# Performance work log

Measured on AMD Instinct MI355X. Metric: run time of the kernel, lower is better.

Reference implementation:

```python
import jax, jax.numpy as jnp
import numpy as np
from jax import lax

# Model config (matches init_kwargs)
D = 256          # input_size
DO = 256         # output_size
H = 512          # hidden_size
E = 8            # num_experts
NB = 4           # num_bands
R = 8            # lora_rank
ALPHA = 16.0     # lora_alpha
CAP_F = 1.25     # capacity_factor
F = 64           # dct_freq_features
N = 65536        # num tokens
CAP = int(CAP_F * N / E)  # 10240 tokens per expert (expert-choice capacity)


def setup_inputs() -> dict:
    key = jax.random.key(0)
    ks = jax.random.split(key, 14)
    s = 0.02
    return {
        "x": jax.random.normal(ks[0], (N, D), jnp.float32),
        "band": jax.random.randint(ks[1], (N,), 0, NB, jnp.int32),
        "W_dct": jax.random.normal(ks[2], (D, F), jnp.float32) * s,
        "W_gate": jax.random.normal(ks[3], (D + F, E), jnp.float32) * s,
        "W1": jax.random.normal(ks[4], (E, D + 1, H), jnp.float32) * s,
        "b1": jnp.zeros((E, H), jnp.float32),
        "A1": jax.random.normal(ks[5], (E, NB, D + 1, R), jnp.float32) * s,
        "B1": jax.random.normal(ks[6], (E, NB, R, H), jnp.float32) * s,
        "W2": jax.random.normal(ks[7], (E, H, DO), jnp.float32) * s,
        "b2": jnp.zeros((E, DO), jnp.float32),
        "A2": jax.random.normal(ks[8], (E, NB, H, R), jnp.float32) * s,
        "B2": jax.random.normal(ks[9], (E, NB, R, DO), jnp.float32) * s,
    }


def reference(x, band, W_dct, W_gate, W1, b1, A1, B1, W2, b2, A2, B2):
    scale = ALPHA / R
    # 1) Frequency-aware gating: concat spatial + (linear) DCT-like features.
    freq = x @ W_dct                                   # [N,F]
    logits = jnp.concatenate([x, freq], -1) @ W_gate   # [N,E]
    # Expert-choice: softmax over the TOKEN axis, each expert picks top-CAP tokens.
    scores = jax.nn.softmax(logits, axis=0)            # [N,E]
    g, idx = lax.top_k(scores.T, CAP)                  # [E,CAP] weights / token ids
    # 2) Dispatch: gather tokens (band scalar appended -> input_size+1 features).
    band_f = band.astype(x.dtype)[:, None] / NB        # [N,1]
    x_full = jnp.concatenate([x, band_f], -1)          # [N,D+1]
    xe = x_full[idx]                                   # [E,CAP,D+1]
    oh = jax.nn.one_hot(band[idx], NB, dtype=x.dtype)  # [E,CAP,NB]
    ohn = jnp.transpose(oh, (0, 2, 1))[..., None]      # [E,NB,CAP,1]
    # 3) Per-expert shared MLP with per-band LoRA adapters (layer 1).
    h = jnp.einsum('ecd,edh->ech', xe, W1) + b1[:, None, :]
    u = jnp.einsum('ecd,endr->encr', xe, A1) * ohn     # band-select low-rank code
    h = h + scale * jnp.einsum('encr,enrh->ech', u, B1)
    h = jax.nn.gelu(h)
    # Layer 2.
    o = jnp.einsum('ech,eho->eco', h, W2) + b2[:, None, :]
    v = jnp.einsum('ech,enhr->encr', h, A2) * ohn
    o = o + scale * jnp.einsum('encr,enro->eco', v, B2)
    # 4) Combine: scatter-add gate-weighted expert outputs (unselected tokens -> 0).
    y = jnp.zeros((N, DO), x.dtype)
    y = y.at[idx.reshape(-1)].add((g[..., None] * o).reshape(-1, DO))
    return y
```

## Files before the change

### kernel.cpp

```cpp
#include <hip/hip_runtime.h>
#include <hip/hip_bf16.h>
#include <math.h>

#define NTOK 65536
#define DIN 256
#define DOUT 256
#define HID 512
#define NEXP 8
#define NBAND 4
#define RANK 8
#define CAP 10240
#define NTILE 64
#define TILES_PER_E (CAP / NTILE)

#define W1CAT_PER_E (34 * 9 * 512)
#define B1CAT_OFF   (NEXP * W1CAT_PER_E)
#define B1CAT_PER_E (32 * 512)
#define W2CAT_OFF   (B1CAT_OFF + NEXP * B1CAT_PER_E)
#define W2CAT_PER_E (18 * 16 * 512)
#define B2CAT_OFF   (W2CAT_OFF + NEXP * W2CAT_PER_E)
#define B2CAT_PER_E (16 * 512)
#define PK_TOTAL    (B2CAT_OFF + NEXP * B2CAT_PER_E)
#define PK_F32_OFF  1200000

typedef short s16x8 __attribute__((ext_vector_type(8)));
typedef float f32x4 __attribute__((ext_vector_type(4)));

__device__ __forceinline__ unsigned key_of(float f) {
    unsigned u = __float_as_uint(f);
    return (u & 0x80000000u) ? ~u : (u | 0x80000000u);
}
__device__ __forceinline__ float gelu_fast(float v) {
    const float c = 0.7978845608028654f;
    float z = c * (v + 0.044715f * v * v * v);
    float e = __expf(2.0f * z);
    return v * (1.0f - __builtin_amdgcn_rcpf(e + 1.0f));
}
__device__ __forceinline__ ushort f2bf(float f) {
    unsigned u = __float_as_uint(f);
    return (ushort)((u + 0x7FFFu + ((u >> 16) & 1u)) >> 16);
}

__global__ __launch_bounds__(256) void k_foldw(const float* __restrict__ Wdct,
                                               const float* __restrict__ Wgate,
                                               float* __restrict__ weff) {
    int d = threadIdx.x;
    float acc[8];
#pragma unroll
    for (int e = 0; e < 8; ++e) acc[e] = Wgate[d * 8 + e];
    for (int f = 0; f < 64; ++f) {
        float wv = Wdct[d * 64 + f];
#pragma unroll
        for (int e = 0; e < 8; ++e) acc[e] += wv * Wgate[(256 + f) * 8 + e];
    }
#pragma unroll
    for (int e = 0; e < 8; ++e) weff[d * 8 + e] = acc[e];
}

__global__ __launch_bounds__(256) void k_logits(const float* __restrict__ x,
                                                const float* __restrict__ weff,
                                                float* __restrict__ logitsT,
                                                float* __restrict__ partials) {
    __shared__ float pr[4][8];
    int tid = threadIdx.x, w = tid >> 6, lane = tid & 63;
    int wid = blockIdx.x * 4 + w;
    int nbase = wid * 16;
    float4 wa[4], wb[4];
#pragma unroll
    for (int j = 0; j < 4; ++j) {
        const float* wr = weff + (lane * 4 + j) * 8;
        wa[j] = *(const float4*)wr;
        wb[j] = *(const float4*)(wr + 4);
    }
    float es = 0.f;
    for (int t = 0; t < 16; ++t) {
        int n = nbase + t;
        float4 v = *(const float4*)(x + (size_t)n * DIN + lane * 4);
        float acc[8];
#pragma unroll
        for (int e = 0; e < 8; ++e) acc[e] = 0.f;
#pragma unroll
        for (int j = 0; j < 4; ++j) {
            float vj = (j == 0) ? v.x : (j == 1) ? v.y : (j == 2) ? v.z : v.w;
            acc[0] += vj * wa[j].x; acc[1] += vj * wa[j].y;
            acc[2] += vj * wa[j].z; acc[3] += vj * wa[j].w;
            acc[4] += vj * wb[j].x; acc[5] += vj * wb[j].y;
            acc[6] += vj * wb[j].z; acc[7] += vj * wb[j].w;
        }
#pragma unroll
        for (int off = 1; off < 64; off <<= 1) {
#pragma unroll
            for (int e = 0; e < 8; ++e) acc[e] += __shfl_xor(acc[e], off);
        }
        float out = acc[0];
#pragma unroll
        for (int e = 1; e < 8; ++e) if (lane == e) out = acc[e];
        if (lane < 8) {
            logitsT[(size_t)lane * NTOK + n] = out;
            es += expf(out);
        }
    }
    if (lane < 8) pr[w][lane] = es;
    __syncthreads();
    if (tid < 8) partials[(size_t)tid * 1024 + blockIdx.x] =
        pr[0][tid] + pr[1][tid] + pr[2][tid] + pr[3][tid];
}

__global__ __launch_bounds__(1024) void k_topk(const float* __restrict__ logitsT,
                                               const float* __restrict__ partials,
                                               float* __restrict__ colsum,
                                               int* __restrict__ idxbuf) {
    __shared__ unsigned subh[16][257];
    __shared__ unsigned bins[256];
    __shared__ float ssum[16];
    __shared__ unsigned sval[2];
    __shared__ unsigned scnt, stcnt;
    __shared__ int ties_l[2048];
    int e = blockIdx.x, tid = threadIdx.x, w = tid >> 6, lane = tid & 63;
    const float* lp = logitsT + (size_t)e * NTOK;

    {
        float s = partials[(size_t)e * 1024 + tid];
#pragma unroll
        for (int off = 32; off > 0; off >>= 1) s += __shfl_xor(s, off);
        if (lane == 0) ssum[w] = s;
        __syncthreads();
        if (tid == 0) {
            float t = 0.f;
#pragma unroll
            for (int i = 0; i < 16; ++i) t += ssum[i];
            colsum[e] = t;
        }
    }

    unsigned pref = 0, rem = CAP;
    for (int p = 0; p < 4; ++p) {
        int shift = 24 - 8 * p;
        for (int i = tid; i < 16 * 257; i += 1024) ((unsigned*)subh)[i] = 0;
        __syncthreads();
        for (int it = 0; it < 64; ++it) {
            int n = it * 1024 + tid;
            unsigned k = key_of(lp[n]);
            bool ok = (p == 0) || ((k >> (shift + 8)) == pref);
            if (ok) atomicAdd(&subh[w][(k >> shift) & 255u], 1u);
        }
        __syncthreads();
        if (tid < 256) {
            unsigned c = 0;
#pragma unroll
            for (int ww = 0; ww < 16; ++ww) c += subh[ww][tid];
            bins[tid] = c;
        }
        __syncthreads();
        for (int off = 1; off < 256; off <<= 1) {
            unsigned add = (tid < 256 && tid + off < 256) ? bins[tid + off] : 0u;
            __syncthreads();
            if (tid < 256) bins[tid] += add;
            __syncthreads();
        }
        if (tid < 256) {
            unsigned snext = (tid == 255) ? 0u : bins[tid + 1];
            if (bins[tid] >= rem && snext < rem) {
                sval[0] = (pref << 8) | (unsigned)tid;
                sval[1] = rem - snext;
            }
        }
        __syncthreads();
        pref = sval[0];
        rem = sval[1];
        __syncthreads();
    }

    if (tid == 0) { scnt = 0; stcnt = 0; }
    __syncthreads();
    unsigned T = pref;
    for (int it = 0; it < 64; ++it) {
        int n = it * 1024 + tid;
        unsigned k = key_of(lp[n]);
        if (k > T) {
            unsigned pos = atomicAdd(&scnt, 1u);
            idxbuf[e * CAP + pos] = n;
        } else if (k == T) {
            unsigned tp = atomicAdd(&stcnt, 1u);
            if (tp < 2048) ties_l[tp] = n;
        }
    }
    __syncthreads();
    int m = (int)stcnt, r = (int)rem, base = CAP - r;
    if (m == r) {
        for (int i = tid; i < m; i += 1024) idxbuf[e * CAP + base + i] = ties_l[i];
    } else {
        for (int i = tid; i < m; i += 1024) {
            int my = ties_l[i];
            int rank = 0;
            for (int j = 0; j < m; ++j) rank += (ties_l[j] < my);
            if (rank < r) idxbuf[e * CAP + base + rank] = my;
        }
    }
}

__global__ __launch_bounds__(256) void k_prep(const float* __restrict__ W1,
                                              const float* __restrict__ A1,
                                              const float* __restrict__ B1,
                                              const float* __restrict__ W2,
                                              const float* __restrict__ A2,
                                              const float* __restrict__ B2,
                                              ushort* __restrict__ pk) {
    int id = blockIdx.x * 256 + threadIdx.x;
    if (id >= PK_TOTAL) return;
    float val;
    if (id < B1CAT_OFF) {
        int e = id / W1CAT_PER_E, rem = id % W1CAT_PER_E;
        int t = rem / (9 * 512); rem %= 9 * 512;
        int s = rem / 512; int q = rem & 511;
        int l = q >> 3, j = q & 7;
        int k = s * 32 + ((l >> 4) << 3) + j;
        int col = t * 16 + (l & 15);
        if (k > 256) val = 0.f;
        else if (col < 512) val = W1[((size_t)e * 257 + k) * 512 + col];
        else {
            int cu = col - 512;
            val = A1[(((size_t)e * NBAND + (cu >> 3)) * 257 + k) * RANK + (cu & 7)];
        }
    } else if (id < W2CAT_OFF) {
        int id2 = id - B1CAT_OFF;
        int e = id2 / B1CAT_PER_E, rem = id2 % B1CAT_PER_E;
        int t = rem / 512; int q = rem & 511;
        int l = q >> 3, j = q & 7;
        int k32 = ((l >> 4) << 3) + j;
        int col = t * 16 + (l & 15);
        val = 2.0f * B1[(((size_t)e * NBAND + (k32 >> 3)) * RANK + (k32 & 7)) * 512 + col];
    } else if (id < B2CAT_OFF) {
        int id2 = id - W2CAT_OFF;
        int e = id2 / W2CAT_PER_E, rem = id2 % W2CAT_PER_E;
        int t = rem / (16 * 512); rem %= 16 * 512;
        int s = rem / 512; int q = rem & 511;
        int l = q >> 3, j = q & 7;
        int k = s * 32 + ((l >> 4) << 3) + j;
        int col = t * 16 + (l & 15);
        if (col < 256) val = W2[((size_t)e * 512 + k) * 256 + col];
        else {
            int cv = col - 256;
            val = A2[(((size_t)e * NBAND + (cv >> 3)) * 512 + k) * RANK + (cv & 7)];
        }
    } else {
        int id2 = id - B2CAT_OFF;
        int e = id2 / B2CAT_PER_E, rem = id2 % B2CAT_PER_E;
        int t = rem / 512; int q = rem & 511;
        int l = q >> 3, j = q & 7;
        int k32 = ((l >> 4) << 3) + j;
        int col = t * 16 + (l & 15);
        val = 2.0f * B2[(((size_t)e * NBAND + (k32 >> 3)) * RANK + (k32 & 7)) * 256 + col];
    }
    pk[id] = f2bf(val);
}

__global__ __launch_bounds__(256, 2) void k_expert(
    const float* __restrict__ x, const int* __restrict__ band,
    const float* __restrict__ b1, const float* __restrict__ b2,
    const ushort* __restrict__ pk,
    const float* __restrict__ logitsT,
    const float* __restrict__ colsum, const int* __restrict__ idxbuf,
    float* __restrict__ y) {
    __shared__ ushort bW1[9216];
    __shared__ ushort bW2[9216];
    __shared__ ushort sc[4][640];
    __shared__ int s_tok[4][16];
    __shared__ int s_band[4][16];
    __shared__ float s_g[4][16];

    int tid = threadIdx.x, w = tid >> 6, lane = tid & 63;
    int bid = blockIdx.x;
    int e = bid & 7;
    int tile = bid >> 3;

    if (lane < 16) {
        int n = idxbuf[e * CAP + tile * NTILE + w * 16 + lane];
        s_tok[w][lane] = n;
        s_band[w][lane] = band[n];
        s_g[w][lane] = expf(logitsT[(size_t)e * NTOK + n]) / colsum[e];
    }

    int l15 = lane & 15, lg = lane >> 4;
    ushort* scw = &sc[w][0];

    s16x8 a1[9];
    {
        int mytok = s_tok[w][l15];
        const float* xrow = x + (size_t)mytok * DIN;
        int kg = lg << 3;
#pragma unroll
        for (int s = 0; s < 8; ++s) {
            float4 p = *(const float4*)&xrow[s * 32 + kg];
            float4 q = *(const float4*)&xrow[s * 32 + kg + 4];
            s16x8 a;
            a[0] = (short)f2bf(p.x); a[1] = (short)f2bf(p.y);
            a[2] = (short)f2bf(p.z); a[3] = (short)f2bf(p.w);
            a[4] = (short)f2bf(q.x); a[5] = (short)f2bf(q.y);
            a[6] = (short)f2bf(q.z); a[7] = (short)f2bf(q.w);
            a1[s] = a;
        }
        s16x8 a = (s16x8)(short)0;
        if (lane < 16) a[0] = (short)f2bf((float)s_band[w][l15] * 0.25f);
        a1[8] = a;
    }

    const ushort* w1base = pk + (size_t)e * W1CAT_PER_E;
    const ushort* b1base = pk + B1CAT_OFF + (size_t)e * B1CAT_PER_E;
    const ushort* w2base = pk + W2CAT_OFF + (size_t)e * W2CAT_PER_E;
    const ushort* b2base = pk + B2CAT_OFF + (size_t)e * B2CAT_PER_E;

    s16x8 stg[9];
    if (w < 2) {
        const ushort* s0 = w2base + (size_t)(w * 9) * 16 * 512 + lane * 8;
#pragma unroll
        for (int i = 0; i < 9; ++i)
            stg[i] = *(const s16x8*)(s0 + (size_t)i * 16 * 512);
    } else {
        const ushort* s0 = w1base + (size_t)(w - 2) * 9 * 512 + lane * 8;
#pragma unroll
        for (int i = 0; i < 9; ++i)
            stg[i] = *(const s16x8*)(s0 + i * 512);
    }

    s16x8 ufrag;
    {
#pragma unroll
        for (int t = 32; t <= 33; ++t) {
            f32x4 acc = {0.f, 0.f, 0.f, 0.f};
#pragma unroll
            for (int s = 0; s < 9; ++s) {
                s16x8 b = *(const s16x8*)(w1base + ((size_t)t * 9 + s) * 512 + lane * 8);
                acc = __builtin_amdgcn_mfma_f32_16x16x32_bf16(a1[s], b, acc, 0, 0, 0);
            }
            int colbase = (t - 32) * 16 + l15;
#pragma unroll
            for (int r = 0; r < 4; ++r) {
                int row = lg * 4 + r;
                float v = ((colbase >> 3) == s_band[w][row]) ? acc[r] : 0.f;
                scw[row * 40 + colbase] = f2bf(v);
            }
        }
        asm volatile("s_waitcnt lgkmcnt(0)" ::: "memory");
        __builtin_amdgcn_sched_barrier(0);
        ufrag = *(const s16x8*)&scw[l15 * 40 + lg * 8];
    }

    f32x4 oacc[16];
#pragma unroll
    for (int t2 = 0; t2 < 16; ++t2) {
        float bv = b2[(size_t)e * DOUT + t2 * 16 + l15];
        oacc[t2] = (f32x4){bv, bv, bv, bv};
    }
    f32x4 vacc[2];
    vacc[0] = (f32x4){0.f, 0.f, 0.f, 0.f};
    vacc[1] = (f32x4){0.f, 0.f, 0.f, 0.f};

    if (w < 2) {
#pragma unroll
        for (int i = 0; i < 9; ++i)
            *(s16x8*)(&bW2[(w * 9 + i) * 512] + lane * 8) = stg[i];
    } else {
#pragma unroll
        for (int i = 0; i < 9; ++i)
            *(s16x8*)(&bW1[((w - 2) * 9 + i) * 512] + lane * 8) = stg[i];
    }
    __syncthreads();

#pragma unroll 1
    for (int p = 0; p < 16; ++p) {
        s16x8 st2[9];
        if (p < 15) {
            int p1 = p + 1;
            if (w < 2) {
                const ushort* s0 = w2base + ((size_t)(w * 9) * 16 + p1) * 512 + lane * 8;
#pragma unroll
                for (int i = 0; i < 9; ++i)
                    st2[i] = *(const s16x8*)(s0 + (size_t)i * 16 * 512);
            } else {
                int t = p1 * 2 + (w - 2);
                const ushort* s0 = w1base + (size_t)t * 9 * 512 + lane * 8;
#pragma unroll
                for (int i = 0; i < 9; ++i)
                    st2[i] = *(const s16x8*)(s0 + i * 512);
            }
        }
#pragma unroll
        for (int half = 0; half < 2; ++half) {
            int t = p * 2 + half;
            float bv = b1[(size_t)e * HID + t * 16 + l15];
            f32x4 acc = {bv, bv, bv, bv};
#pragma unroll
            for (int s = 0; s < 9; ++s) {
                s16x8 b = *(const s16x8*)(&bW1[(half * 9 + s) * 512] + lane * 8);
                acc = __builtin_amdgcn_mfma_f32_16x16x32_bf16(a1[s], b, acc, 0, 0, 0);
            }
            {
                s16x8 b = *(const s16x8*)(b1base + (size_t)t * 512 + lane * 8);
                acc = __builtin_amdgcn_mfma_f32_16x16x32_bf16(ufrag, b, acc, 0, 0, 0);
            }
#pragma unroll
            for (int r = 0; r < 4; ++r) {
                int row = lg * 4 + r;
                scw[row * 40 + half * 16 + l15] = f2bf(gelu_fast(acc[r]));
            }
        }
        asm volatile("s_waitcnt lgkmcnt(0)" ::: "memory");
        __builtin_amdgcn_sched_barrier(0);
        s16x8 hfrag = *(const s16x8*)&scw[l15 * 40 + lg * 8];
#pragma unroll
        for (int t2 = 0; t2 < 16; ++t2) {
            s16x8 b = *(const s16x8*)(&bW2[t2 * 512] + lane * 8);
            oacc[t2] = __builtin_amdgcn_mfma_f32_16x16x32_bf16(hfrag, b, oacc[t2], 0, 0, 0);
        }
#pragma unroll
        for (int i = 0; i < 2; ++i) {
            s16x8 b = *(const s16x8*)(&bW2[(16 + i) * 512] + lane * 8);
            vacc[i] = __builtin_amdgcn_mfma_f32_16x16x32_bf16(hfrag, b, vacc[i], 0, 0, 0);
        }
        if (p < 15) {
            __syncthreads();
            if (w < 2) {
#pragma unroll
                for (int i = 0; i < 9; ++i)
                    *(s16x8*)(&bW2[(w * 9 + i) * 512] + lane * 8) = st2[i];
            } else {
#pragma unroll
                for (int i = 0; i < 9; ++i)
                    *(s16x8*)(&bW1[((w - 2) * 9 + i) * 512] + lane * 8) = st2[i];
            }
            __syncthreads();
        }
    }

    s16x8 vfrag;
    {
#pragma unroll
        for (int i = 0; i < 2; ++i) {
            int colbase = i * 16 + l15;
#pragma unroll
            for (int r = 0; r < 4; ++r) {
                int row = lg * 4 + r;
                float v = ((colbase >> 3) == s_band[w][row]) ? vacc[i][r] : 0.f;
                scw[row * 40 + colbase] = f2bf(v);
            }
        }
        asm volatile("s_waitcnt lgkmcnt(0)" ::: "memory");
        __builtin_amdgcn_sched_barrier(0);
        vfrag = *(const s16x8*)&scw[l15 * 40 + lg * 8];
    }

    float g4[4];
    int tok4[4];
#pragma unroll
    for (int r = 0; r < 4; ++r) {
        int row = lg * 4 + r;
        g4[r] = s_g[w][row];
        tok4[r] = s_tok[w][row];
    }
#pragma unroll
    for (int t2 = 0; t2 < 16; ++t2) {
        s16x8 b = *(const s16x8*)(b2base + (size_t)t2 * 512 + lane * 8);
        f32x4 acc = __builtin_amdgcn_mfma_f32_16x16x32_bf16(vfrag, b, oacc[t2], 0, 0, 0);
        int col = t2 * 16 + l15;
#pragma unroll
        for (int r = 0; r < 4; ++r) {
            atomicAdd(&y[(size_t)tok4[r] * DOUT + col], g4[r] * acc[r]);
        }
    }
}

extern "C" void kernel_launch(void* const* d_in, const int* in_sizes, int n_in,
                              void* d_out, int out_size, void* d_ws, size_t ws_size,
                              hipStream_t stream) {
    const float* x = (const float*)d_in[0];
    const int* band = (const int*)d_in[1];
    const float* Wdct = (const float*)d_in[2];
    const float* Wgate = (const float*)d_in[3];
    const float* W1 = (const float*)d_in[4];
    const float* b1 = (const float*)d_in[5];
    const float* A1 = (const float*)d_in[6];
    const float* B1 = (const float*)d_in[7];
    const float* W2 = (const float*)d_in[8];
    const float* b2 = (const float*)d_in[9];
    const float* A2 = (const float*)d_in[10];
    const float* B2 = (const float*)d_in[11];
    float* y = (float*)d_out;

    float* ws = (float*)d_ws;
    float* logitsT = ws;
    float* partials = ws + 524288;
    float* colsum = ws + 532480;
    float* weff = ws + 532488;
    int* idxbuf = (int*)(ws + 534536);
    ushort* pk = (ushort*)(ws + PK_F32_OFF);

    hipMemsetAsync(d_out, 0, (size_t)NTOK * DOUT * sizeof(float), stream);

    k_prep<<<(PK_TOTAL + 255) / 256, 256, 0, stream>>>(W1, A1, B1, W2, A2, B2, pk);
    k_foldw<<<1, 256, 0, stream>>>(Wdct, Wgate, weff);
    k_logits<<<1024, 256, 0, stream>>>(x, weff, logitsT, partials);
    k_topk<<<NEXP, 1024, 0, stream>>>(logitsT, partials, colsum, idxbuf);
    k_expert<<<NEXP * TILES_PER_E, 256, 0, stream>>>(x, band, b1, b2, pk,
                                                     logitsT, colsum, idxbuf, y);
}
```

Before: 300.0 us.

## Fuse weight folding, output zeroing and weight packing into fewer kernel launches

Folds the gating weight product into every k_logits block, which each recompute it into shared memory, and zeroes the output tile from inside k_logits instead of a separate memset. Weight packing (k_prep) is merged into the top-k kernel as extra blocks so it runs alongside the 8 top-k blocks. This cuts the launch count from five plus a memset to three. It also drops the explicit lgkmcnt waits and scheduling barriers before the LDS fragment reads in the expert kernel. The redundant weff computation in each of 1024 blocks adds work, and removing the waits relies on the compiler inserting the correct LDS synchronisation.

```diff
diff --git a/kernel.cpp b/kernel.cpp
--- a/kernel.cpp
+++ b/kernel.cpp
@@ -41,37 +41,45 @@
     return (ushort)((u + 0x7FFFu + ((u >> 16) & 1u)) >> 16);
 }
 
-__global__ __launch_bounds__(256) void k_foldw(const float* __restrict__ Wdct,
-                                               const float* __restrict__ Wgate,
-                                               float* __restrict__ weff) {
-    int d = threadIdx.x;
-    float acc[8];
-#pragma unroll
-    for (int e = 0; e < 8; ++e) acc[e] = Wgate[d * 8 + e];
-    for (int f = 0; f < 64; ++f) {
-        float wv = Wdct[d * 64 + f];
-#pragma unroll
-        for (int e = 0; e < 8; ++e) acc[e] += wv * Wgate[(256 + f) * 8 + e];
-    }
-#pragma unroll
-    for (int e = 0; e < 8; ++e) weff[d * 8 + e] = acc[e];
-}
-
 __global__ __launch_bounds__(256) void k_logits(const float* __restrict__ x,
-                                                const float* __restrict__ weff,
+                                                const float* __restrict__ Wdct,
+                                                const float* __restrict__ Wgate,
                                                 float* __restrict__ logitsT,
-                                                float* __restrict__ partials) {
+                                                float* __restrict__ partials,
+                                                float* __restrict__ y) {
+    __shared__ float wefft[8][257];
     __shared__ float pr[4][8];
     int tid = threadIdx.x, w = tid >> 6, lane = tid & 63;
+
+    {
+        int d = tid;
+        float acc[8];
+#pragma unroll
+        for (int e = 0; e < 8; ++e) acc[e] = Wgate[d * 8 + e];
+        for (int f = 0; f < 64; ++f) {
+            float wv = Wdct[d * 64 + f];
+#pragma unroll
+            for (int e = 0; e < 8; ++e) acc[e] += wv * Wgate[(256 + f) * 8 + e];
+        }
+#pragma unroll
+        for (int e = 0; e < 8; ++e) wefft[e][d] = acc[e];
+    }
+
+    {
+        float4 z = {0.f, 0.f, 0.f, 0.f};
+        float4* yp = (float4*)(y + (size_t)blockIdx.x * 64 * DOUT);
+        for (int i = tid; i < 4096; i += 256) yp[i] = z;
+    }
+    __syncthreads();
+
+    float wje[4][8];
+#pragma unroll
+    for (int j = 0; j < 4; ++j)
+#pragma unroll
+        for (int e = 0; e < 8; ++e) wje[j][e] = wefft[e][lane * 4 + j];
+
     int wid = blockIdx.x * 4 + w;
     int nbase = wid * 16;
-    float4 wa[4], wb[4];
-#pragma unroll
-    for (int j = 0; j < 4; ++j) {
-        const float* wr = weff + (lane * 4 + j) * 8;
-        wa[j] = *(const float4*)wr;
-        wb[j] = *(const float4*)(wr + 4);
-    }
     float es = 0.f;
     for (int t = 0; t < 16; ++t) {
         int n = nbase + t;
@@ -82,10 +90,8 @@
 #pragma unroll
         for (int j = 0; j < 4; ++j) {
             float vj = (j == 0) ? v.x : (j == 1) ? v.y : (j == 2) ? v.z : v.w;
-            acc[0] += vj * wa[j].x; acc[1] += vj * wa[j].y;
-            acc[2] += vj * wa[j].z; acc[3] += vj * wa[j].w;
-            acc[4] += vj * wb[j].x; acc[5] += vj * wb[j].y;
-            acc[6] += vj * wb[j].z; acc[7] += vj * wb[j].w;
+#pragma unroll
+            for (int e = 0; e < 8; ++e) acc[e] += vj * wje[j][e];
         }
 #pragma unroll
         for (int off = 1; off < 64; off <<= 1) {
@@ -106,10 +112,67 @@
         pr[0][tid] + pr[1][tid] + pr[2][tid] + pr[3][tid];
 }
 
-__global__ __launch_bounds__(1024) void k_topk(const float* __restrict__ logitsT,
+__global__ __launch_bounds__(1024) void k_misc(const float* __restrict__ logitsT,
                                                const float* __restrict__ partials,
                                                float* __restrict__ colsum,
-                                               int* __restrict__ idxbuf) {
+                                               int* __restrict__ idxbuf,
+                                               const float* __restrict__ W1,
+                                               const float* __restrict__ A1,
+                                               const float* __restrict__ B1,
+                                               const float* __restrict__ W2,
+                                               const float* __restrict__ A2,
+                                               const float* __restrict__ B2,
+                                               ushort* __restrict__ pk) {
+    if (blockIdx.x >= 8) {
+        int id = (blockIdx.x - 8) * 1024 + threadIdx.x;
+        if (id >= PK_TOTAL) return;
+        float val;
+        if (id < B1CAT_OFF) {
+            int e = id / W1CAT_PER_E, rem = id % W1CAT_PER_E;
+            int t = rem / (9 * 512); rem %= 9 * 512;
+            int s = rem / 512; int q = rem & 511;
+            int l = q >> 3, j = q & 7;
+            int k = s * 32 + ((l >> 4) << 3) + j;
+            int col = t * 16 + (l & 15);
+            if (k > 256) val = 0.f;
+            else if (col < 512) val = W1[((size_t)e * 257 + k) * 512 + col];
+            else {
+                int cu = col - 512;
+                val = A1[(((size_t)e * NBAND + (cu >> 3)) * 257 + k) * RANK + (cu & 7)];
+            }
+        } else if (id < W2CAT_OFF) {
+            int id2 = id - B1CAT_OFF;
+            int e = id2 / B1CAT_PER_E, rem = id2 % B1CAT_PER_E;
+            int t = rem / 512; int q = rem & 511;
+            int l = q >> 3, j = q & 7;
+            int k32 = ((l >> 4) << 3) + j;
+            int col = t * 16 + (l & 15);
+            val = 2.0f * B1[(((size_t)e * NBAND + (k32 >> 3)) * RANK + (k32 & 7)) * 512 + col];
+        } else if (id < B2CAT_OFF) {
+            int id2 = id - W2CAT_OFF;
+            int e = id2 / W2CAT_PER_E, rem = id2 % W2CAT_PER_E;
+            int t = rem / (16 * 512); rem %= 16 * 512;
+            int s = rem / 512; int q = rem & 511;
+            int l = q >> 3, j = q & 7;
+            int k = s * 32 + ((l >> 4) << 3) + j;
+            int col = t * 16 + (l & 15);
+            if (col < 256) val = W2[((size_t)e * 512 + k) * 256 + col];
+            else {
+                int cv = col - 256;
+                val = A2[(((size_t)e * NBAND + (cv >> 3)) * 512 + k) * RANK + (cv & 7)];
+            }
+        } else {
+            int id2 = id - B2CAT_OFF;
+            int e = id2 / B2CAT_PER_E, rem = id2 % B2CAT_PER_E;
+            int t = rem / 512; int q = rem & 511;
+            int l = q >> 3, j = q & 7;
+            int k32 = ((l >> 4) << 3) + j;
+            int col = t * 16 + (l & 15);
+            val = 2.0f * B2[(((size_t)e * NBAND + (k32 >> 3)) * RANK + (k32 & 7)) * 256 + col];
+        }
+        pk[id] = f2bf(val);
+        return;
+    }
     __shared__ unsigned subh[16][257];
     __shared__ unsigned bins[256];
     __shared__ float ssum[16];
@@ -197,62 +260,6 @@
             if (rank < r) idxbuf[e * CAP + base + rank] = my;
         }
     }
-}
-
-__global__ __launch_bounds__(256) void k_prep(const float* __restrict__ W1,
-                                              const float* __restrict__ A1,
-                                              const float* __restrict__ B1,
-                                              const float* __restrict__ W2,
-                                              const float* __restrict__ A2,
-                                              const float* __restrict__ B2,
-                                              ushort* __restrict__ pk) {
-    int id = blockIdx.x * 256 + threadIdx.x;
-    if (id >= PK_TOTAL) return;
-    float val;
-    if (id < B1CAT_OFF) {
-        int e = id / W1CAT_PER_E, rem = id % W1CAT_PER_E;
-        int t = rem / (9 * 512); rem %= 9 * 512;
-        int s = rem / 512; int q = rem & 511;
-        int l = q >> 3, j = q & 7;
-        int k = s * 32 + ((l >> 4) << 3) + j;
-        int col = t * 16 + (l & 15);
-        if (k > 256) val = 0.f;
-        else if (col < 512) val = W1[((size_t)e * 257 + k) * 512 + col];
-        else {
-            int cu = col - 512;
-            val = A1[(((size_t)e * NBAND + (cu >> 3)) * 257 + k) * RANK + (cu & 7)];
-        }
-    } else if (id < W2CAT_OFF) {
-        int id2 = id - B1CAT_OFF;
-        int e = id2 / B1CAT_PER_E, rem = id2 % B1CAT_PER_E;
-        int t = rem / 512; int q = rem & 511;
-        int l = q >> 3, j = q & 7;
-        int k32 = ((l >> 4) << 3) + j;
-        int col = t * 16 + (l & 15);
-        val = 2.0f * B1[(((size_t)e * NBAND + (k32 >> 3)) * RANK + (k32 & 7)) * 512 + col];
-    } else if (id < B2CAT_OFF) {
-        int id2 = id - W2CAT_OFF;
-        int e = id2 / W2CAT_PER_E, rem = id2 % W2CAT_PER_E;
-        int t = rem / (16 * 512); rem %= 16 * 512;
-        int s = rem / 512; int q = rem & 511;
-        int l = q >> 3, j = q & 7;
-        int k = s * 32 + ((l >> 4) << 3) + j;
-        int col = t * 16 + (l & 15);
-        if (col < 256) val = W2[((size_t)e * 512 + k) * 256 + col];
-        else {
-            int cv = col - 256;
-            val = A2[(((size_t)e * NBAND + (cv >> 3)) * 512 + k) * RANK + (cv & 7)];
-        }
-    } else {
-        int id2 = id - B2CAT_OFF;
-        int e = id2 / B2CAT_PER_E, rem = id2 % B2CAT_PER_E;
-        int t = rem / 512; int q = rem & 511;
-        int l = q >> 3, j = q & 7;
-        int k32 = ((l >> 4) << 3) + j;
-        int col = t * 16 + (l & 15);
-        val = 2.0f * B2[(((size_t)e * NBAND + (k32 >> 3)) * RANK + (k32 & 7)) * 256 + col];
-    }
-    pk[id] = f2bf(val);
 }
 
 __global__ __launch_bounds__(256, 2) void k_expert(
@@ -341,8 +348,6 @@
                 scw[row * 40 + colbase] = f2bf(v);
             }
         }
-        asm volatile("s_waitcnt lgkmcnt(0)" ::: "memory");
-        __builtin_amdgcn_sched_barrier(0);
         ufrag = *(const s16x8*)&scw[l15 * 40 + lg * 8];
     }
 
@@ -405,8 +410,6 @@
                 scw[row * 40 + half * 16 + l15] = f2bf(gelu_fast(acc[r]));
             }
         }
-        asm volatile("s_waitcnt lgkmcnt(0)" ::: "memory");
-        __builtin_amdgcn_sched_barrier(0);
         s16x8 hfrag = *(const s16x8*)&scw[l15 * 40 + lg * 8];
 #pragma unroll
         for (int t2 = 0; t2 < 16; ++t2) {
@@ -445,8 +448,6 @@
                 scw[row * 40 + colbase] = f2bf(v);
             }
         }
-        asm volatile("s_waitcnt lgkmcnt(0)" ::: "memory");
-        __builtin_amdgcn_sched_barrier(0);
         vfrag = *(const s16x8*)&scw[l15 * 40 + lg * 8];
     }
 
@@ -491,16 +492,13 @@
     float* logitsT = ws;
     float* partials = ws + 524288;
     float* colsum = ws + 532480;
-    float* weff = ws + 532488;
-    int* idxbuf = (int*)(ws + 534536);
+    int* idxbuf = (int*)(ws + 532488);
     ushort* pk = (ushort*)(ws + PK_F32_OFF);
 
-    hipMemsetAsync(d_out, 0, (size_t)NTOK * DOUT * sizeof(float), stream);
-
-    k_prep<<<(PK_TOTAL + 255) / 256, 256, 0, stream>>>(W1, A1, B1, W2, A2, B2, pk);
-    k_foldw<<<1, 256, 0, stream>>>(Wdct, Wgate, weff);
-    k_logits<<<1024, 256, 0, stream>>>(x, weff, logitsT, partials);
-    k_topk<<<NEXP, 1024, 0, stream>>>(logitsT, partials, colsum, idxbuf);
+    k_logits<<<1024, 256, 0, stream>>>(x, Wdct, Wgate, logitsT, partials, y);
+    k_misc<<<8 + PK_TOTAL / 1024, 1024, 0, stream>>>(logitsT, partials, colsum,
+                                                     idxbuf, W1, A1, B1, W2, A2,
+                                                     B2, pk);
     k_expert<<<NEXP * TILES_PER_E, 256, 0, stream>>>(x, band, b1, b2, pk,
                                                      logitsT, colsum, idxbuf, y);
 }
```

After: 287.7 us, median of 2. 4.1% less time.
